# Kernel optimization log

Hardware: AMD Instinct MI355X
Metric: run time of the kernel (lower is better)

The kernel has to match this reference:

```python
import jax, jax.numpy as jnp
import numpy as np
from jax import lax

B, N, C = 256, 128, 256
GRID_SIZE = 0.05
# eta/phi are sampled in [0, 2), so (v - min)/0.05 < 40 -> grid index <= 39.
# Using a static 40x40 grid is mathematically identical to the dynamic
# H = max+1, W = max+1 of the original: extra rows/cols are zero, which
# matches the 'same' zero padding the depthwise conv would see anyway,
# and gathered positions are unchanged.
HMAX, WMAX = 40, 40
KH = KW = 3


def setup_inputs() -> dict:
    key = jax.random.key(0)
    ks = jax.random.split(key, 9)
    x = jax.random.normal(ks[0], (B, N, C), jnp.float32)
    eta = jax.random.uniform(ks[1], (B, N), jnp.float32, 0.0, 2.0)
    phi = jax.random.uniform(ks[2], (B, N), jnp.float32, 0.0, 2.0)
    # depthwise conv kernel, HWIO with I = in_channels/groups = 1
    conv_kernel = jax.random.normal(ks[3], (KH, KW, 1, C), jnp.float32) * 0.1
    conv_bias = jax.random.normal(ks[4], (C,), jnp.float32) * 0.01
    dense_w = jax.random.normal(ks[5], (C, C), jnp.float32) * (1.0 / np.sqrt(C))
    dense_b = jax.random.normal(ks[6], (C,), jnp.float32) * 0.01
    gamma = jnp.ones((C,), jnp.float32)
    beta = jnp.zeros((C,), jnp.float32)
    return {
        "x": x, "eta": eta, "phi": phi,
        "conv_kernel": conv_kernel, "conv_bias": conv_bias,
        "dense_w": dense_w, "dense_b": dense_b,
        "gamma": gamma, "beta": beta,
    }


def reference(x, eta, phi, conv_kernel, conv_bias, dense_w, dense_b, gamma, beta):
    Bq, Nq, Cq = x.shape
    # quantize particle positions to grid bins (per-batch min shift)
    ge = ((eta - eta.min(axis=1, keepdims=True)) / GRID_SIZE).astype(jnp.int32)  # [B,N]
    gp = ((phi - phi.min(axis=1, keepdims=True)) / GRID_SIZE).astype(jnp.int32)  # [B,N]
    b_idx = jnp.arange(Bq)[:, None]  # broadcasts against [B,N]

    # scatter-add particle features into dense (eta,phi) grid
    grid = jnp.zeros((Bq, HMAX, WMAX, Cq), x.dtype).at[b_idx, ge, gp].add(x)

    # depthwise 3x3 conv, 'same' zero padding, per-channel bias
    grid = lax.conv_general_dilated(
        grid, conv_kernel, window_strides=(1, 1), padding="SAME",
        dimension_numbers=("NHWC", "HWIO", "NHWC"), feature_group_count=Cq,
    ) + conv_bias

    # gather back to particles
    out = grid[b_idx, ge, gp]  # [B, N, C]

    # pointwise dense
    out = jnp.einsum("bnc,cd->bnd", out, dense_w) + dense_b

    # layer norm (eps=1e-6, biased variance, channel affine)
    mean = out.mean(axis=-1, keepdims=True)
    var = jnp.mean(jnp.square(out - mean), axis=-1, keepdims=True)
    out = (out - mean) * lax.rsqrt(var + 1e-6) * gamma + beta

    return x + out
```

## Files before the change

### kernel.cpp

```cpp
#include <hip/hip_runtime.h>

typedef __attribute__((ext_vector_type(8))) short bf16x8;
typedef __attribute__((ext_vector_type(4))) float f32x4;

#define Bq 256
#define Nq 128
#define Cq 256
#define TP 16
#define NBLK (Nq / TP)

__device__ __forceinline__ unsigned short f2bf(float f) {
    unsigned int u = __float_as_uint(f);
    u += 0x7fffu + ((u >> 16) & 1u);
    return (unsigned short)(u >> 16);
}

struct ushort4_t { unsigned short x, y, z, w; };

__device__ __forceinline__ void fma4(float4& a, const float4& k, const float4& x) {
    a.x = fmaf(k.x, x.x, a.x);
    a.y = fmaf(k.y, x.y, a.y);
    a.z = fmaf(k.z, x.z, a.z);
    a.w = fmaf(k.w, x.w, a.w);
}

__global__ __launch_bounds__(256) void wpack_kernel(const float* __restrict__ dw,
                                                    unsigned short* __restrict__ wp) {
    int tid = blockIdx.x * 256 + threadIdx.x;
    int j    = tid & 7;
    int lane = (tid >> 3) & 63;
    int nt   = (tid >> 9) & 15;
    int kt   = tid >> 13;
    int k = kt * 32 + (lane >> 4) * 8 + j;
    int n = nt * 16 + (lane & 15);
    wp[tid] = f2bf(dw[k * Cq + n]);
}

__global__ __launch_bounds__(256, 4) void fused_kernel(
    const float* __restrict__ x, const float* __restrict__ eta, const float* __restrict__ phi,
    const float* __restrict__ ck, const float* __restrict__ cb,
    const unsigned short* __restrict__ wp, const float* __restrict__ db,
    const float* __restrict__ gamma, const float* __restrict__ beta,
    float* __restrict__ out) {
    const int b  = blockIdx.x >> 3;
    const int p0 = (blockIdx.x & (NBLK - 1)) * TP;
    const int t  = threadIdx.x;
    const int lane = t & 63, wave = t >> 6;

    __shared__ int   s_ge[Nq], s_gp[Nq];
    __shared__ float s_ck[10 * Cq];
    __shared__ float s_min[4];
    __shared__ int   s_cnt[TP];
    __shared__ unsigned short s_list[TP][132];
    __shared__ unsigned short s_A[8 * 64 * 8] __attribute__((aligned(16)));
    __shared__ float s_sum[TP][4], s_sq[TP][4];

    float ev = 0.f, pv = 0.f;
    if (t < Nq) {
        ev = eta[b * Nq + t];
        pv = phi[b * Nq + t];
        float emin = ev, pmin = pv;
#pragma unroll
        for (int off = 32; off > 0; off >>= 1) {
            emin = fminf(emin, __shfl_down(emin, off));
            pmin = fminf(pmin, __shfl_down(pmin, off));
        }
        if ((t & 63) == 0) { s_min[wave] = emin; s_min[2 + wave] = pmin; }
    }
#pragma unroll
    for (int i = t; i < 9 * Cq; i += 256) s_ck[i] = ck[i];
    s_ck[9 * Cq + t] = 0.0f;
    if (t < TP) s_cnt[t] = 0;
    __syncthreads();

    if (t < Nq) {
        float Emin = fminf(s_min[0], s_min[1]);
        float Pmin = fminf(s_min[2], s_min[3]);
        s_ge[t] = (int)((ev - Emin) / 0.05f);
        s_gp[t] = (int)((pv - Pmin) / 0.05f);
    }
    __syncthreads();

    const int pp = t >> 4, cg = t & 15;

    {
        int th = s_ge[p0 + pp], tw = s_gp[p0 + pp];
#pragma unroll
        for (int i = 0; i < 8; ++i) {
            int m = cg * 8 + i;
            int dh = s_ge[m] - th, dv = s_gp[m] - tw;
            if (dh >= -1 && dh <= 1 && dv >= -1 && dv <= 1) {
                int k = (dh + 1) * 3 + (dv + 1);
                int pos = atomicAdd(&s_cnt[pp], 1);
                s_list[pp][pos] = (unsigned short)(m | (k << 7));
            }
        }
    }
    __syncthreads();
    if (t < TP) {
        int c = s_cnt[t];
        if (c & 1) { s_list[t][c] = (unsigned short)(9 << 7); s_cnt[t] = c + 1; }
    }
    __syncthreads();

    {
        const float4* x4  = (const float4*)x + (size_t)b * (Nq * Cq / 4) + cg;
        const float4* ck4 = (const float4*)s_ck + cg;
        const float4* cb4 = (const float4*)cb + cg;
        float4 a0 = cb4[0], a1 = cb4[16], a2 = cb4[32], a3 = cb4[48];

        const int cnt = s_cnt[pp];
        const unsigned short* lst = s_list[pp];
        for (int i = 0; i < cnt; i += 2) {
            int e0 = lst[i], e1 = lst[i + 1];
            const float4* xp0 = x4  + ((e0 & 127) << 6);
            const float4* kp0 = ck4 + ((e0 >> 7)  << 6);
            const float4* xp1 = x4  + ((e1 & 127) << 6);
            const float4* kp1 = ck4 + ((e1 >> 7)  << 6);
            float4 X00 = xp0[0], X01 = xp0[16], X02 = xp0[32], X03 = xp0[48];
            float4 X10 = xp1[0], X11 = xp1[16], X12 = xp1[32], X13 = xp1[48];
            float4 K00 = kp0[0], K01 = kp0[16], K02 = kp0[32], K03 = kp0[48];
            float4 K10 = kp1[0], K11 = kp1[16], K12 = kp1[32], K13 = kp1[48];
            fma4(a0, K00, X00); fma4(a1, K01, X01);
            fma4(a2, K02, X02); fma4(a3, K03, X03);
            fma4(a0, K10, X10); fma4(a1, K11, X11);
            fma4(a2, K12, X12); fma4(a3, K13, X13);
        }

        const int g = (cg >> 1) & 3;
        const int lidx = ((pp + 2 * g) & 15) | (g << 4);
        const int off = (cg & 1) * 4;
        float4 aj[4] = {a0, a1, a2, a3};
#pragma unroll
        for (int j = 0; j < 4; ++j) {
            int kt = j * 2 + (cg >> 3);
            ushort4_t v;
            v.x = f2bf(aj[j].x); v.y = f2bf(aj[j].y);
            v.z = f2bf(aj[j].z); v.w = f2bf(aj[j].w);
            *(ushort4_t*)&s_A[(kt * 64 + lidx) * 8 + off] = v;
        }
    }
    __syncthreads();

    f32x4 acc[4];
#pragma unroll
    for (int ntl = 0; ntl < 4; ++ntl) acc[ntl] = (f32x4){0.f, 0.f, 0.f, 0.f};

    const int g2 = lane >> 4, m2 = lane & 15;
    const int alidx = ((m2 + 2 * g2) & 15) | (g2 << 4);
#pragma unroll
    for (int kt2 = 0; kt2 < 8; ++kt2) {
        bf16x8 af = *reinterpret_cast<const bf16x8*>(&s_A[(kt2 * 64 + alidx) * 8]);
#pragma unroll
        for (int ntl = 0; ntl < 4; ++ntl) {
            int nt = wave * 4 + ntl;
            bf16x8 bfr = *reinterpret_cast<const bf16x8*>(&wp[((kt2 * 16 + nt) * 64 + lane) * 8]);
            acc[ntl] = __builtin_amdgcn_mfma_f32_16x16x32_bf16(af, bfr, acc[ntl], 0, 0, 0);
        }
    }

    float dbv[4], gv[4], bv[4];
#pragma unroll
    for (int ntl = 0; ntl < 4; ++ntl) {
        int col = (wave * 4 + ntl) * 16 + m2;
        dbv[ntl] = db[col]; gv[ntl] = gamma[col]; bv[ntl] = beta[col];
    }
#pragma unroll
    for (int r = 0; r < 4; ++r) {
        float a = 0.f, q = 0.f;
#pragma unroll
        for (int ntl = 0; ntl < 4; ++ntl) {
            float y = acc[ntl][r] + dbv[ntl];
            a += y; q += y * y;
        }
#pragma unroll
        for (int off = 8; off >= 1; off >>= 1) {
            a += __shfl_xor(a, off);
            q += __shfl_xor(q, off);
        }
        if (m2 == 0) {
            int row = g2 * 4 + r;
            s_sum[row][wave] = a;
            s_sq[row][wave]  = q;
        }
    }
    __syncthreads();

#pragma unroll
    for (int r = 0; r < 4; ++r) {
        int row = g2 * 4 + r;
        float s = s_sum[row][0] + s_sum[row][1] + s_sum[row][2] + s_sum[row][3];
        float q = s_sq[row][0] + s_sq[row][1] + s_sq[row][2] + s_sq[row][3];
        float mean = s * (1.0f / Cq);
        float var  = q * (1.0f / Cq) - mean * mean;
        float inv  = rsqrtf(var + 1e-6f);
        int gbase = (b * Nq + p0 + row) * Cq + wave * 64 + m2;
#pragma unroll
        for (int ntl = 0; ntl < 4; ++ntl) {
            float y = acc[ntl][r] + dbv[ntl];
            int idx = gbase + ntl * 16;
            out[idx] = x[idx] + (y - mean) * inv * gv[ntl] + bv[ntl];
        }
    }
}

extern "C" void kernel_launch(void* const* d_in, const int* in_sizes, int n_in,
                              void* d_out, int out_size, void* d_ws, size_t ws_size,
                              hipStream_t stream) {
    const float* x     = (const float*)d_in[0];
    const float* eta   = (const float*)d_in[1];
    const float* phi   = (const float*)d_in[2];
    const float* ck    = (const float*)d_in[3];
    const float* cb    = (const float*)d_in[4];
    const float* dw    = (const float*)d_in[5];
    const float* db    = (const float*)d_in[6];
    const float* gamma = (const float*)d_in[7];
    const float* beta  = (const float*)d_in[8];
    float* out = (float*)d_out;

    unsigned short* wpk = (unsigned short*)d_ws;

    wpack_kernel<<<Cq, 256, 0, stream>>>(dw, wpk);
    fused_kernel<<<Bq * NBLK, 256, 0, stream>>>(x, eta, phi, ck, cb, wpk, db,
                                                gamma, beta, out);
}
```

Measured before the change: 119.5 us.

## Drop block-wide barriers; compute grid bins per wave and share them with bpermute

Each wave now loads all 128 eta/phi values, reduces the per-batch minima with xor shuffles, and fetches neighbour bin indices through ds_bpermute instead of LDS arrays. Each particle's neighbour list is built and consumed entirely within one wave, so the block barriers are replaced by block fences. The conv kernel is read from global memory (cache) instead of being staged in LDS, which frees about 10KB of LDS per block and may raise occupancy. The odd-count padding entry is replaced by a scalar tail iteration. In exchange the min reduction is done redundantly in every wave, there are many more bpermute ops in the neighbour search, and correctness now relies on wave-local lockstep ordering.

```diff
diff --git a/kernel.cpp b/kernel.cpp
--- a/kernel.cpp
+++ b/kernel.cpp
@@ -47,48 +47,47 @@
     const int t  = threadIdx.x;
     const int lane = t & 63, wave = t >> 6;
 
-    __shared__ int   s_ge[Nq], s_gp[Nq];
-    __shared__ float s_ck[10 * Cq];
-    __shared__ float s_min[4];
     __shared__ int   s_cnt[TP];
     __shared__ unsigned short s_list[TP][132];
     __shared__ unsigned short s_A[8 * 64 * 8] __attribute__((aligned(16)));
     __shared__ float s_sum[TP][4], s_sq[TP][4];
 
-    float ev = 0.f, pv = 0.f;
-    if (t < Nq) {
-        ev = eta[b * Nq + t];
-        pv = phi[b * Nq + t];
-        float emin = ev, pmin = pv;
-#pragma unroll
-        for (int off = 32; off > 0; off >>= 1) {
-            emin = fminf(emin, __shfl_down(emin, off));
-            pmin = fminf(pmin, __shfl_down(pmin, off));
-        }
-        if ((t & 63) == 0) { s_min[wave] = emin; s_min[2 + wave] = pmin; }
-    }
-#pragma unroll
-    for (int i = t; i < 9 * Cq; i += 256) s_ck[i] = ck[i];
-    s_ck[9 * Cq + t] = 0.0f;
-    if (t < TP) s_cnt[t] = 0;
-    __syncthreads();
-
-    if (t < Nq) {
-        float Emin = fminf(s_min[0], s_min[1]);
-        float Pmin = fminf(s_min[2], s_min[3]);
-        s_ge[t] = (int)((ev - Emin) / 0.05f);
-        s_gp[t] = (int)((pv - Pmin) / 0.05f);
-    }
-    __syncthreads();
-
     const int pp = t >> 4, cg = t & 15;
 
+    float e0 = eta[b * Nq + lane], e1 = eta[b * Nq + 64 + lane];
+    float q0 = phi[b * Nq + lane], q1 = phi[b * Nq + 64 + lane];
+    float emin = fminf(e0, e1), pmin = fminf(q0, q1);
+#pragma unroll
+    for (int off = 32; off > 0; off >>= 1) {
+        emin = fminf(emin, __shfl_xor(emin, off));
+        pmin = fminf(pmin, __shfl_xor(pmin, off));
+    }
+    int ge0 = (int)((e0 - emin) / 0.05f), ge1 = (int)((e1 - emin) / 0.05f);
+    int gp0 = (int)((q0 - pmin) / 0.05f), gp1 = (int)((q1 - pmin) / 0.05f);
+
+    if ((lane >> 4) == 0) s_cnt[4 * wave + (lane & 3)] = 0;
+    __threadfence_block();
+
     {
-        int th = s_ge[p0 + pp], tw = s_gp[p0 + pp];
+        int P = p0 + pp;
+        int pa = (P & 63) << 2;
+        int tel = __builtin_amdgcn_ds_bpermute(pa, ge0);
+        int teh = __builtin_amdgcn_ds_bpermute(pa, ge1);
+        int tpl = __builtin_amdgcn_ds_bpermute(pa, gp0);
+        int tph = __builtin_amdgcn_ds_bpermute(pa, gp1);
+        int th = (P < 64) ? tel : teh;
+        int tw = (P < 64) ? tpl : tph;
 #pragma unroll
         for (int i = 0; i < 8; ++i) {
             int m = cg * 8 + i;
-            int dh = s_ge[m] - th, dv = s_gp[m] - tw;
+            int ma = (m & 63) << 2;
+            int mel = __builtin_amdgcn_ds_bpermute(ma, ge0);
+            int meh = __builtin_amdgcn_ds_bpermute(ma, ge1);
+            int mpl = __builtin_amdgcn_ds_bpermute(ma, gp0);
+            int mph = __builtin_amdgcn_ds_bpermute(ma, gp1);
+            int me = (m < 64) ? mel : meh;
+            int mp = (m < 64) ? mpl : mph;
+            int dh = me - th, dv = mp - tw;
             if (dh >= -1 && dh <= 1 && dv >= -1 && dv <= 1) {
                 int k = (dh + 1) * 3 + (dv + 1);
                 int pos = atomicAdd(&s_cnt[pp], 1);
@@ -96,27 +95,23 @@
             }
         }
     }
-    __syncthreads();
-    if (t < TP) {
-        int c = s_cnt[t];
-        if (c & 1) { s_list[t][c] = (unsigned short)(9 << 7); s_cnt[t] = c + 1; }
-    }
-    __syncthreads();
+    __threadfence_block();
 
     {
         const float4* x4  = (const float4*)x + (size_t)b * (Nq * Cq / 4) + cg;
-        const float4* ck4 = (const float4*)s_ck + cg;
+        const float4* ck4 = (const float4*)ck + cg;
         const float4* cb4 = (const float4*)cb + cg;
         float4 a0 = cb4[0], a1 = cb4[16], a2 = cb4[32], a3 = cb4[48];
 
         const int cnt = s_cnt[pp];
         const unsigned short* lst = s_list[pp];
-        for (int i = 0; i < cnt; i += 2) {
-            int e0 = lst[i], e1 = lst[i + 1];
-            const float4* xp0 = x4  + ((e0 & 127) << 6);
-            const float4* kp0 = ck4 + ((e0 >> 7)  << 6);
-            const float4* xp1 = x4  + ((e1 & 127) << 6);
-            const float4* kp1 = ck4 + ((e1 >> 7)  << 6);
+        int i = 0;
+        for (; i + 2 <= cnt; i += 2) {
+            int e0_ = lst[i], e1_ = lst[i + 1];
+            const float4* xp0 = x4  + ((e0_ & 127) << 6);
+            const float4* kp0 = ck4 + ((e0_ >> 7)  << 6);
+            const float4* xp1 = x4  + ((e1_ & 127) << 6);
+            const float4* kp1 = ck4 + ((e1_ >> 7)  << 6);
             float4 X00 = xp0[0], X01 = xp0[16], X02 = xp0[32], X03 = xp0[48];
             float4 X10 = xp1[0], X11 = xp1[16], X12 = xp1[32], X13 = xp1[48];
             float4 K00 = kp0[0], K01 = kp0[16], K02 = kp0[32], K03 = kp0[48];
@@ -125,6 +120,15 @@
             fma4(a2, K02, X02); fma4(a3, K03, X03);
             fma4(a0, K10, X10); fma4(a1, K11, X11);
             fma4(a2, K12, X12); fma4(a3, K13, X13);
+        }
+        if (i < cnt) {
+            int e0_ = lst[i];
+            const float4* xp0 = x4  + ((e0_ & 127) << 6);
+            const float4* kp0 = ck4 + ((e0_ >> 7)  << 6);
+            float4 X00 = xp0[0], X01 = xp0[16], X02 = xp0[32], X03 = xp0[48];
+            float4 K00 = kp0[0], K01 = kp0[16], K02 = kp0[32], K03 = kp0[48];
+            fma4(a0, K00, X00); fma4(a1, K01, X01);
+            fma4(a2, K02, X02); fma4(a3, K03, X03);
         }
 
         const int g = (cg >> 1) & 3;
```

Result: no change. 117.2 us (-1.9%).
